# Performance work log

Measured on AMD Instinct MI355X. Metric: run time of the kernel, lower is better.

## Reference

```python
import jax, jax.numpy as jnp
import numpy as np
import math

NUM_BUCKETS = 32
MAX_DISTANCE = 128


def _relative_position_buckets(seq_len):
    # bidirectional T5-style buckets, matching the torch reference exactly
    pos = jnp.arange(seq_len)
    rp = pos[None, :] - pos[:, None]                # [S, S]
    nb = NUM_BUCKETS // 2                            # bidirectional halving
    buckets = (rp > 0).astype(jnp.int32) * nb
    rp = jnp.abs(rp)
    max_exact = nb // 2
    is_small = rp < max_exact
    rp_f = jnp.maximum(rp, 1).astype(jnp.float32)    # avoid log(0); masked by is_small
    rp_large = max_exact + (
        jnp.log(rp_f / max_exact) / math.log(MAX_DISTANCE / max_exact) * (nb - max_exact)
    ).astype(jnp.int32)                              # trunc toward zero, like .to(torch.long)
    rp_large = jnp.minimum(rp_large, nb - 1)
    return buckets + jnp.where(is_small, rp, rp_large)  # [S, S] int32 in [0, 31]


def setup_inputs() -> dict:
    key = jax.random.key(0)
    kq, kk, kv, km, kb = jax.random.split(key, 5)
    B, H, S, D = 4, 4, 2048, 64
    return {
        "query": jax.random.normal(kq, (B, H, S, D), dtype=jnp.float32),
        "key": jax.random.normal(kk, (B, H, S, D), dtype=jnp.float32),
        "value": jax.random.normal(kv, (B, H, S, D), dtype=jnp.float32),
        "mask": jax.random.randint(km, (B, 1, 1, S), 0, 2, dtype=jnp.int32),
        "bias_table": jax.random.normal(kb, (512, 4), dtype=jnp.float32) * 0.02,
    }


def reference(query, key, value, mask, bias_table):
    B, H, S, D = query.shape
    attn = jnp.einsum("bhqd,bhkd->bhqk", query, key)          # [B,H,S,S]
    rel = _relative_position_buckets(S)                        # [S,S]
    bias = bias_table[rel]                                     # [S,S,H]
    bias = jnp.transpose(bias, (2, 0, 1))[None]                # [1,H,S,S]
    scores = (attn + bias) / math.sqrt(D)                      # bias added pre-scale, as in torch
    scores = jnp.where(mask == 0, jnp.float32(-1e9), scores)
    p_attn = jax.nn.softmax(scores, axis=-1)
    out = jnp.einsum("bhqk,bhkd->bhqd", p_attn, value)
    return out, p_attn
```

## Files before the change

### kernel.cpp

```cpp
#include <hip/hip_runtime.h>
#include <math.h>

typedef __attribute__((ext_vector_type(4))) float f32x4;
typedef _Float16 f16x8 __attribute__((ext_vector_type(8)));
typedef _Float16 f16x4v __attribute__((ext_vector_type(4)));

#define S_LEN 2048
#define D_HEAD 64
#define C2 0.18033688011112043f

static __device__ __forceinline__ float exp2v(float x) {
    float r; asm("v_exp_f32 %0, %1" : "=v"(r) : "v"(x)); return r;
}

static __device__ __forceinline__ void gl_lds16(const void* g, void* l) {
    __builtin_amdgcn_global_load_lds(
        (const __attribute__((address_space(1))) unsigned int*)g,
        (__attribute__((address_space(3))) unsigned int*)l, 16, 0, 0);
}

__global__ void prep_bias(const float* __restrict__ table, float* __restrict__ bias_d) {
    int idx = blockIdx.x * blockDim.x + threadIdx.x;
    if (idx >= 4096) return;
    int delta = idx - 2047;
    int bpos = (delta > 0) ? 16 : 0;
    int ad = delta < 0 ? -delta : delta;
    int rel;
    if (ad < 8) {
        rel = bpos + ad;
    } else {
        float rp = (float)ad;
        int lg = 8 + (int)(logf(rp / 8.0f) / 2.772588722239781f * 8.0f);
        if (lg > 15) lg = 15;
        rel = bpos + lg;
    }
    #pragma unroll
    for (int h = 0; h < 4; ++h)
        bias_d[h * 4096 + idx] = C2 * table[rel * 4 + h];
}

__global__ void prep_half(const float* __restrict__ src, _Float16* __restrict__ dst) {
    size_t i8 = ((size_t)blockIdx.x * 256 + threadIdx.x) * 8;
    f32x4 a = *(const f32x4*)(src + i8);
    f32x4 b = *(const f32x4*)(src + i8 + 4);
    f16x8 h;
    h[0] = (_Float16)a[0]; h[1] = (_Float16)a[1];
    h[2] = (_Float16)a[2]; h[3] = (_Float16)a[3];
    h[4] = (_Float16)b[0]; h[5] = (_Float16)b[1];
    h[6] = (_Float16)b[2]; h[7] = (_Float16)b[3];
    *(f16x8*)(dst + i8) = h;
}

__global__ void prep_vt(const float* __restrict__ V, _Float16* __restrict__ vt) {
    __shared__ float tile[64][65];
    const int bh = blockIdx.y;
    const int k0 = blockIdx.x * 64;
    const int t = threadIdx.x;
    {
        int r = t >> 2, c0 = (t & 3) * 16;
        const float* src = V + ((size_t)bh * S_LEN + k0 + r) * D_HEAD + c0;
        #pragma unroll
        for (int i = 0; i < 16; i += 4) {
            f32x4 v = *(const f32x4*)(src + i);
            tile[r][c0 + i + 0] = v[0];
            tile[r][c0 + i + 1] = v[1];
            tile[r][c0 + i + 2] = v[2];
            tile[r][c0 + i + 3] = v[3];
        }
    }
    __syncthreads();
    {
        int d = t >> 2, kc = (t & 3) * 16;
        size_t ob = ((size_t)bh * D_HEAD + d) * S_LEN + k0 + kc;
        #pragma unroll
        for (int half = 0; half < 2; ++half) {
            f16x8 hv;
            #pragma unroll
            for (int i = 0; i < 8; ++i)
                hv[i] = (_Float16)tile[kc + half * 8 + i][d];
            *(f16x8*)(vt + ob + half * 8) = hv;
        }
    }
}

__launch_bounds__(512, 6)
__global__ void attn_main(const float* __restrict__ Q, const int* __restrict__ mask,
                          const float* __restrict__ bias2,
                          const _Float16* __restrict__ kh_g,
                          const _Float16* __restrict__ vt_g,
                          float* __restrict__ outp, float* __restrict__ p_out) {
    __shared__ __align__(16) char smem[53760];
    _Float16* pball = (_Float16*)(smem + 32768);
    float* stats = (float*)(smem + 53248);

    const int tid = threadIdx.x;
    const int w = tid >> 6, l = tid & 63;
    const int wq = w & 3, wk = w >> 2;
    const int g = l >> 4, lq = l & 15;
    const int r7 = lq & 7;
    const int bid = blockIdx.x;
    const int bh = bid & 15, b = bh >> 2, h = bh & 3;
    const int q0 = (bid >> 4) * 64;

    const float* Qp = Q + (size_t)bh * (S_LEN * D_HEAD);
    const int* mp = mask + b * S_LEN;
    const _Float16* khp = kh_g + (size_t)bh * (S_LEN * D_HEAD);
    const _Float16* vhp = vt_g + (size_t)bh * (S_LEN * D_HEAD);

    _Float16* qarea = (_Float16*)smem;
    {
        int sr = tid >> 3, tb = tid & 7;
        const float* src = Qp + (size_t)(q0 + sr) * D_HEAD + tb * 8;
        f32x4 a = *(const f32x4*)src;
        f32x4 c = *(const f32x4*)(src + 4);
        f16x8 hv;
        hv[0] = (_Float16)a[0]; hv[1] = (_Float16)a[1];
        hv[2] = (_Float16)a[2]; hv[3] = (_Float16)a[3];
        hv[4] = (_Float16)c[0]; hv[5] = (_Float16)c[1];
        hv[6] = (_Float16)c[2]; hv[7] = (_Float16)c[3];
        *(f16x8*)(qarea + sr * 64 + ((tb ^ (sr & 7)) * 8)) = hv;
    }
    __syncthreads();
    f16x8 qf[2];
    const int qrow = 16 * wq + lq;
    #pragma unroll
    for (int c = 0; c < 2; ++c)
        qf[c] = *(const f16x8*)(qarea + qrow * 64 + ((4 * c + g) ^ r7) * 8);
    __syncthreads();

    const int qq = q0 + qrow;

    const int rr3 = tid >> 3;
    const int ub0 = (((tid & 7) ^ (rr3 & 7)) * 8);
    const _Float16* s1a = khp + (size_t)rr3 * 64 + ub0;
    gl_lds16(s1a, smem + tid * 16);
    gl_lds16(s1a + 4096, smem + 8192 + tid * 16);
    __syncthreads();

    const int* mP1 = mp + 64 * wk + 4 * g;
    const float* bP1 = bias2 + h * 4096 + 2047 - qq + 64 * wk + 4 * g;
    float lsum = 0.0f;
    for (int t = 0; t < 16; ++t) {
        const char* kb = smem + (t & 1) * 16384;
        int4 mv[4]; f32x4 bv[4];
        #pragma unroll
        for (int t2 = 0; t2 < 4; ++t2) {
            mv[t2] = *(const int4*)(mP1 + 16 * t2);
            bv[t2] = *(const f32x4*)(bP1 + 16 * t2);
        }
        if (t < 15) {
            s1a += 8192;
            char* nb = smem + ((t + 1) & 1) * 16384 + tid * 16;
            gl_lds16(s1a, nb);
            gl_lds16(s1a + 4096, nb + 8192);
        }
        __builtin_amdgcn_sched_barrier(0);
        #pragma unroll
        for (int t2 = 0; t2 < 4; ++t2) {
            const int krow = 64 * wk + 16 * t2 + lq;
            f32x4 acc = {0.f, 0.f, 0.f, 0.f};
            #pragma unroll
            for (int c = 0; c < 2; ++c) {
                f16x8 af = *(const f16x8*)(kb + krow * 128 + ((4 * c + g) ^ r7) * 16);
                acc = __builtin_amdgcn_mfma_f32_16x16x32_f16(af, qf[c], acc, 0, 0, 0);
            }
            float s0 = mv[t2].x ? fmaf(acc[0], C2, bv[t2][0]) : -1e9f;
            float s1 = mv[t2].y ? fmaf(acc[1], C2, bv[t2][1]) : -1e9f;
            float s2 = mv[t2].z ? fmaf(acc[2], C2, bv[t2][2]) : -1e9f;
            float s3 = mv[t2].w ? fmaf(acc[3], C2, bv[t2][3]) : -1e9f;
            lsum += exp2v(s0) + exp2v(s1) + exp2v(s2) + exp2v(s3);
        }
        mP1 += 128; bP1 += 128;
        asm volatile("s_waitcnt vmcnt(0)" ::: "memory");
        __builtin_amdgcn_sched_barrier(0);
        __builtin_amdgcn_s_barrier();
        __builtin_amdgcn_sched_barrier(0);
    }
    lsum += __shfl_xor(lsum, 16);
    lsum += __shfl_xor(lsum, 32);
    if (g == 0) stats[wk * 64 + qrow] = lsum;

    const _Float16* sKh = khp + (size_t)rr3 * 64 + ub0;
    const _Float16* sVh = vhp + (size_t)rr3 * 2048 + ub0;
    gl_lds16(sKh, smem + tid * 16);
    gl_lds16(sVh, smem + 8192 + tid * 16);
    __syncthreads();
    float lr2q;
    {
        float L = stats[qrow] + stats[64 + qrow];
        float lg; asm("v_log_f32 %0, %1" : "=v"(lg) : "v"(L));
        lr2q = -lg;
    }

    f32x4 acco[4] = {{0.f,0.f,0.f,0.f},{0.f,0.f,0.f,0.f},{0.f,0.f,0.f,0.f},{0.f,0.f,0.f,0.f}};
    const int* mP = mp + 32 * wk + 4 * g;
    const float* bP = bias2 + h * 4096 + 2047 - qq + 32 * wk + 4 * g;
    const int kAoff0 = (32 * wk + lq) * 128;
    const int voffb = lq * 128 + ((4 * wk + g) ^ r7) * 16;
    _Float16* pwr = pball + w * 1280 + lq * 40 + g * 4;
    const _Float16* prd = pball + w * 1280 + lq * 40 + g * 8;
    const _Float16* flb = pball + ((((l >> 3) & 1) * 4 + wq) * 1280)
                        + (8 * wk + (l >> 4)) * 40 + (l & 7) * 4;
    float* pF = p_out + (size_t)bh * (S_LEN * S_LEN)
              + (size_t)(q0 + 16 * wq + 8 * wk + (l >> 4)) * S_LEN + (l & 15) * 4;

    for (int t = 0; t < 32; ++t) {
        const int cb = (t & 1) * 16384;
        const int cs = (t & 1) * 640;
        int4 mv[2]; f32x4 bv[2];
        #pragma unroll
        for (int t2 = 0; t2 < 2; ++t2) {
            mv[t2] = *(const int4*)(mP + 16 * t2);
            bv[t2] = *(const f32x4*)(bP + 16 * t2);
        }
        if (t < 31) {
            sKh += 4096; sVh += 64;
            char* d0 = smem + ((t + 1) & 1) * 16384 + tid * 16;
            gl_lds16(sKh, d0);
            gl_lds16(sVh, d0 + 8192);
        }
        if (t > 0) {
            const int ps = cs ^ 640;
            #pragma unroll
            for (int i = 0; i < 2; ++i) {
                f16x4v v = *(const f16x4v*)(flb + ps + i * 160);
                f32x4 wv;
                wv[0] = (float)v[0]; wv[1] = (float)v[1];
                wv[2] = (float)v[2]; wv[3] = (float)v[3];
                *(f32x4*)(pF + (size_t)(4 * i) * S_LEN) = wv;
            }
            pF += 64;
        }
        __builtin_amdgcn_sched_barrier(0);
        #pragma unroll
        for (int t2 = 0; t2 < 2; ++t2) {
            const char* kbase = smem + cb + kAoff0 + t2 * 2048;
            f32x4 acc = {0.f, 0.f, 0.f, 0.f};
            #pragma unroll
            for (int c = 0; c < 2; ++c) {
                f16x8 ah = *(const f16x8*)(kbase + ((4 * c + g) ^ r7) * 16);
                acc = __builtin_amdgcn_mfma_f32_16x16x32_f16(ah, qf[c], acc, 0, 0, 0);
            }
            float p0 = exp2v(mv[t2].x ? fmaf(acc[0], C2, bv[t2][0]) + lr2q : -1e9f);
            float p1 = exp2v(mv[t2].y ? fmaf(acc[1], C2, bv[t2][1]) + lr2q : -1e9f);
            float p2 = exp2v(mv[t2].z ? fmaf(acc[2], C2, bv[t2][2]) + lr2q : -1e9f);
            float p3 = exp2v(mv[t2].w ? fmaf(acc[3], C2, bv[t2][3]) + lr2q : -1e9f);
            f16x4v ph;
            ph[0] = (_Float16)p0; ph[1] = (_Float16)p1;
            ph[2] = (_Float16)p2; ph[3] = (_Float16)p3;
            *(f16x4v*)(pwr + cs + 16 * t2) = ph;
        }
        const f16x8 pf = *(const f16x8*)(prd + cs);
        #pragma unroll
        for (int n = 0; n < 4; ++n) {
            const f16x8 bhf = *(const f16x8*)(smem + cb + 8192 + voffb + n * 2048);
            acco[n] = __builtin_amdgcn_mfma_f32_16x16x32_f16(pf, bhf, acco[n], 0, 0, 0);
        }
        mP += 64; bP += 64;
        asm volatile("s_waitcnt vmcnt(2) lgkmcnt(0)" ::: "memory");
        __builtin_amdgcn_sched_barrier(0);
        __builtin_amdgcn_s_barrier();
        __builtin_amdgcn_sched_barrier(0);
    }
    {
        #pragma unroll
        for (int i = 0; i < 2; ++i) {
            f16x4v v = *(const f16x4v*)(flb + 640 + i * 160);
            f32x4 wv;
            wv[0] = (float)v[0]; wv[1] = (float)v[1];
            wv[2] = (float)v[2]; wv[3] = (float)v[3];
            *(f32x4*)(pF + (size_t)(4 * i) * S_LEN) = wv;
        }
    }

    float* ored = (float*)smem;
    __syncthreads();
    if (wk == 1) {
        #pragma unroll
        for (int n = 0; n < 4; ++n)
            #pragma unroll
            for (int r = 0; r < 4; ++r)
                ored[(wq * 16 + 4 * g + r) * 64 + 16 * n + lq] = acco[n][r];
    }
    __syncthreads();
    if (wk == 0) {
        #pragma unroll
        for (int n = 0; n < 4; ++n) {
            #pragma unroll
            for (int r = 0; r < 4; ++r) {
                float v = acco[n][r] + ored[(wq * 16 + 4 * g + r) * 64 + 16 * n + lq];
                outp[((size_t)bh * S_LEN + q0 + 16 * wq + 4 * g + r) * D_HEAD + 16 * n + lq] = v;
            }
        }
    }
}

extern "C" void kernel_launch(void* const* d_in, const int* in_sizes, int n_in,
                              void* d_out, int out_size, void* d_ws, size_t ws_size,
                              hipStream_t stream) {
    const float* Q = (const float*)d_in[0];
    const float* K = (const float*)d_in[1];
    const float* V = (const float*)d_in[2];
    const int* mask = (const int*)d_in[3];
    const float* table = (const float*)d_in[4];

    float* outp = (float*)d_out;
    float* p_out = outp + (size_t)4 * 4 * 2048 * 64;

    float* bias_d = (float*)d_ws;
    _Float16* kh = (_Float16*)((char*)d_ws + 65536);
    _Float16* vt = kh + (size_t)16 * S_LEN * D_HEAD;

    prep_bias<<<16, 256, 0, stream>>>(table, bias_d);
    prep_half<<<1024, 256, 0, stream>>>(K, kh);
    prep_vt<<<dim3(32, 16), 256, 0, stream>>>(V, vt);
    attn_main<<<512, 512, 0, stream>>>(Q, mask, bias_d, kh, vt, outp, p_out);
}
```

Measured before the change: 92.69 us.

## Merge prep kernels into one launch and double the pass-1 key tile

Folds the three preprocessing kernels (bias table, K half conversion, V transpose) into a single launch, selecting the role by block index, to cut launch overhead and inter-kernel gaps. The first pass of the attention kernel now stages 256 key rows per iteration instead of 128, halving its barrier and loop count. Shared memory grows to about 66 KB and the occupancy hint drops from 6 to 4, so fewer blocks may be resident per CU.

Result: slower. 97.31 us (+5.0%).

```diff
diff --git a/kernel.cpp b/kernel.cpp
--- a/kernel.cpp
+++ b/kernel.cpp
@@ -19,79 +19,83 @@
         (__attribute__((address_space(3))) unsigned int*)l, 16, 0, 0);
 }
 
-__global__ void prep_bias(const float* __restrict__ table, float* __restrict__ bias_d) {
-    int idx = blockIdx.x * blockDim.x + threadIdx.x;
-    if (idx >= 4096) return;
-    int delta = idx - 2047;
-    int bpos = (delta > 0) ? 16 : 0;
-    int ad = delta < 0 ? -delta : delta;
-    int rel;
-    if (ad < 8) {
-        rel = bpos + ad;
+__global__ void prep_all(const float* __restrict__ K, const float* __restrict__ V,
+                         const float* __restrict__ table,
+                         _Float16* __restrict__ kh, _Float16* __restrict__ vt,
+                         float* __restrict__ bias_d) {
+    __shared__ float tile[64][65];
+    const int bid = blockIdx.x;
+    const int t = threadIdx.x;
+    if (bid < 1024) {
+        size_t i8 = ((size_t)bid * 256 + t) * 8;
+        f32x4 a = *(const f32x4*)(K + i8);
+        f32x4 b = *(const f32x4*)(K + i8 + 4);
+        f16x8 h;
+        h[0] = (_Float16)a[0]; h[1] = (_Float16)a[1];
+        h[2] = (_Float16)a[2]; h[3] = (_Float16)a[3];
+        h[4] = (_Float16)b[0]; h[5] = (_Float16)b[1];
+        h[6] = (_Float16)b[2]; h[7] = (_Float16)b[3];
+        *(f16x8*)(kh + i8) = h;
+    } else if (bid < 1536) {
+        const int vb = bid - 1024;
+        const int bh = vb >> 5;
+        const int k0 = (vb & 31) * 64;
+        {
+            int r = t >> 2, c0 = (t & 3) * 16;
+            const float* src = V + ((size_t)bh * S_LEN + k0 + r) * D_HEAD + c0;
+            #pragma unroll
+            for (int i = 0; i < 16; i += 4) {
+                f32x4 v = *(const f32x4*)(src + i);
+                tile[r][c0 + i + 0] = v[0];
+                tile[r][c0 + i + 1] = v[1];
+                tile[r][c0 + i + 2] = v[2];
+                tile[r][c0 + i + 3] = v[3];
+            }
+        }
+        __syncthreads();
+        {
+            int d = t >> 2, kc = (t & 3) * 16;
+            size_t ob = ((size_t)bh * D_HEAD + d) * S_LEN + k0 + kc;
+            #pragma unroll
+            for (int half = 0; half < 2; ++half) {
+                f16x8 hv;
+                #pragma unroll
+                for (int i = 0; i < 8; ++i)
+                    hv[i] = (_Float16)tile[kc + half * 8 + i][d];
+                *(f16x8*)(vt + ob + half * 8) = hv;
+            }
+        }
     } else {
-        float rp = (float)ad;
-        int lg = 8 + (int)(logf(rp / 8.0f) / 2.772588722239781f * 8.0f);
-        if (lg > 15) lg = 15;
-        rel = bpos + lg;
-    }
-    #pragma unroll
-    for (int h = 0; h < 4; ++h)
-        bias_d[h * 4096 + idx] = C2 * table[rel * 4 + h];
-}
-
-__global__ void prep_half(const float* __restrict__ src, _Float16* __restrict__ dst) {
-    size_t i8 = ((size_t)blockIdx.x * 256 + threadIdx.x) * 8;
-    f32x4 a = *(const f32x4*)(src + i8);
-    f32x4 b = *(const f32x4*)(src + i8 + 4);
-    f16x8 h;
-    h[0] = (_Float16)a[0]; h[1] = (_Float16)a[1];
-    h[2] = (_Float16)a[2]; h[3] = (_Float16)a[3];
-    h[4] = (_Float16)b[0]; h[5] = (_Float16)b[1];
-    h[6] = (_Float16)b[2]; h[7] = (_Float16)b[3];
-    *(f16x8*)(dst + i8) = h;
-}
-
-__global__ void prep_vt(const float* __restrict__ V, _Float16* __restrict__ vt) {
-    __shared__ float tile[64][65];
-    const int bh = blockIdx.y;
-    const int k0 = blockIdx.x * 64;
-    const int t = threadIdx.x;
-    {
-        int r = t >> 2, c0 = (t & 3) * 16;
-        const float* src = V + ((size_t)bh * S_LEN + k0 + r) * D_HEAD + c0;
-        #pragma unroll
-        for (int i = 0; i < 16; i += 4) {
-            f32x4 v = *(const f32x4*)(src + i);
-            tile[r][c0 + i + 0] = v[0];
-            tile[r][c0 + i + 1] = v[1];
-            tile[r][c0 + i + 2] = v[2];
-            tile[r][c0 + i + 3] = v[3];
-        }
-    }
-    __syncthreads();
-    {
-        int d = t >> 2, kc = (t & 3) * 16;
-        size_t ob = ((size_t)bh * D_HEAD + d) * S_LEN + k0 + kc;
-        #pragma unroll
-        for (int half = 0; half < 2; ++half) {
-            f16x8 hv;
-            #pragma unroll
-            for (int i = 0; i < 8; ++i)
-                hv[i] = (_Float16)tile[kc + half * 8 + i][d];
-            *(f16x8*)(vt + ob + half * 8) = hv;
-        }
-    }
-}
-
-__launch_bounds__(512, 6)
+        int idx = (bid - 1536) * 256 + t;
+        if (idx < 4096) {
+            int delta = idx - 2047;
+            int bpos = (delta > 0) ? 16 : 0;
+            int ad = delta < 0 ? -delta : delta;
+            int rel;
+            if (ad < 8) {
+                rel = bpos + ad;
+            } else {
+                float rp = (float)ad;
+                int lg = 8 + (int)(logf(rp / 8.0f) / 2.772588722239781f * 8.0f);
+                if (lg > 15) lg = 15;
+                rel = bpos + lg;
+            }
+            #pragma unroll
+            for (int hh = 0; hh < 4; ++hh)
+                bias_d[hh * 4096 + idx] = C2 * table[rel * 4 + hh];
+        }
+    }
+}
+
+__launch_bounds__(512, 4)
 __global__ void attn_main(const float* __restrict__ Q, const int* __restrict__ mask,
                           const float* __restrict__ bias2,
                           const _Float16* __restrict__ kh_g,
                           const _Float16* __restrict__ vt_g,
                           float* __restrict__ outp, float* __restrict__ p_out) {
-    __shared__ __align__(16) char smem[53760];
+    __shared__ __align__(16) char smem[66048];
     _Float16* pball = (_Float16*)(smem + 32768);
-    float* stats = (float*)(smem + 53248);
+    float* stats = (float*)(smem + 65536);
 
     const int tid = threadIdx.x;
     const int w = tid >> 6, l = tid & 63;
@@ -133,31 +137,35 @@
     const int rr3 = tid >> 3;
     const int ub0 = (((tid & 7) ^ (rr3 & 7)) * 8);
     const _Float16* s1a = khp + (size_t)rr3 * 64 + ub0;
-    gl_lds16(s1a, smem + tid * 16);
-    gl_lds16(s1a + 4096, smem + 8192 + tid * 16);
-    __syncthreads();
-
-    const int* mP1 = mp + 64 * wk + 4 * g;
-    const float* bP1 = bias2 + h * 4096 + 2047 - qq + 64 * wk + 4 * g;
+    gl_lds16(s1a,          smem + tid * 16);
+    gl_lds16(s1a + 4096,   smem + 8192  + tid * 16);
+    gl_lds16(s1a + 8192,   smem + 16384 + tid * 16);
+    gl_lds16(s1a + 12288,  smem + 24576 + tid * 16);
+    __syncthreads();
+
+    const int* mP1 = mp + 128 * wk + 4 * g;
+    const float* bP1 = bias2 + h * 4096 + 2047 - qq + 128 * wk + 4 * g;
     float lsum = 0.0f;
-    for (int t = 0; t < 16; ++t) {
-        const char* kb = smem + (t & 1) * 16384;
-        int4 mv[4]; f32x4 bv[4];
-        #pragma unroll
-        for (int t2 = 0; t2 < 4; ++t2) {
+    for (int t = 0; t < 8; ++t) {
+        const char* kb = smem + (t & 1) * 32768;
+        int4 mv[8]; f32x4 bv[8];
+        #pragma unroll
+        for (int t2 = 0; t2 < 8; ++t2) {
             mv[t2] = *(const int4*)(mP1 + 16 * t2);
             bv[t2] = *(const f32x4*)(bP1 + 16 * t2);
         }
-        if (t < 15) {
-            s1a += 8192;
-            char* nb = smem + ((t + 1) & 1) * 16384 + tid * 16;
+        if (t < 7) {
+            s1a += 16384;
+            char* nb = smem + ((t + 1) & 1) * 32768 + tid * 16;
             gl_lds16(s1a, nb);
             gl_lds16(s1a + 4096, nb + 8192);
-        }
-        __builtin_amdgcn_sched_barrier(0);
-        #pragma unroll
-        for (int t2 = 0; t2 < 4; ++t2) {
-            const int krow = 64 * wk + 16 * t2 + lq;
+            gl_lds16(s1a + 8192, nb + 16384);
+            gl_lds16(s1a + 12288, nb + 24576);
+        }
+        __builtin_amdgcn_sched_barrier(0);
+        #pragma unroll
+        for (int t2 = 0; t2 < 8; ++t2) {
+            const int krow = 128 * wk + 16 * t2 + lq;
             f32x4 acc = {0.f, 0.f, 0.f, 0.f};
             #pragma unroll
             for (int c = 0; c < 2; ++c) {
@@ -170,7 +178,7 @@
             float s3 = mv[t2].w ? fmaf(acc[3], C2, bv[t2][3]) : -1e9f;
             lsum += exp2v(s0) + exp2v(s1) + exp2v(s2) + exp2v(s3);
         }
-        mP1 += 128; bP1 += 128;
+        mP1 += 256; bP1 += 256;
         asm volatile("s_waitcnt vmcnt(0)" ::: "memory");
         __builtin_amdgcn_sched_barrier(0);
         __builtin_amdgcn_s_barrier();
@@ -311,8 +319,6 @@
     _Float16* kh = (_Float16*)((char*)d_ws + 65536);
     _Float16* vt = kh + (size_t)16 * S_LEN * D_HEAD;
 
-    prep_bias<<<16, 256, 0, stream>>>(table, bias_d);
-    prep_half<<<1024, 256, 0, stream>>>(K, kh);
-    prep_vt<<<dim3(32, 16), 256, 0, stream>>>(V, vt);
+    prep_all<<<1552, 256, 0, stream>>>(K, V, table, kh, vt, bias_d);
     attn_main<<<512, 512, 0, stream>>>(Q, mask, bias_d, kh, vt, outp, p_out);
 }
```
